# Performance work log

Measured on AMD Instinct MI355X. Metric: run time of the kernel, lower is better.

The kernel has to match this reference:

```python
import jax, jax.numpy as jnp
import numpy as np

N_NODES = 20000
IN_DIM = 256
HID = 128
N_CLASSES = 64
N_EDGES = 320000
EPS_BN = 1e-5


def setup_inputs() -> dict:
    key = jax.random.key(0)
    ks = jax.random.split(key, 24)
    s = 0.1
    inp = {}
    inp['x'] = jax.random.normal(ks[0], (N_NODES, IN_DIM), dtype=jnp.float32)
    inp['edge_index'] = jax.random.randint(ks[1], (2, N_EDGES), 0, N_NODES, dtype=jnp.int32)
    # GATConv 1: in=IN_DIM, out=HID per head, heads=4, concat=False
    inp['W1'] = s * jax.random.normal(ks[2], (IN_DIM, 4 * HID), dtype=jnp.float32)
    inp['a_src1'] = s * jax.random.normal(ks[3], (4, HID), dtype=jnp.float32)
    inp['a_dst1'] = s * jax.random.normal(ks[4], (4, HID), dtype=jnp.float32)
    inp['b1'] = jnp.zeros((HID,), jnp.float32)
    # GATConv 2: in=HID, out=HID per head, heads=4, concat=False
    inp['W2'] = s * jax.random.normal(ks[5], (HID, 4 * HID), dtype=jnp.float32)
    inp['a_src2'] = s * jax.random.normal(ks[6], (4, HID), dtype=jnp.float32)
    inp['a_dst2'] = s * jax.random.normal(ks[7], (4, HID), dtype=jnp.float32)
    inp['b2'] = jnp.zeros((HID,), jnp.float32)
    # GATConv 3: heads=1, concat=True (default)
    inp['W3'] = s * jax.random.normal(ks[8], (HID, HID), dtype=jnp.float32)
    inp['a_src3'] = s * jax.random.normal(ks[9], (1, HID), dtype=jnp.float32)
    inp['a_dst3'] = s * jax.random.normal(ks[10], (1, HID), dtype=jnp.float32)
    inp['b3'] = jnp.zeros((HID,), jnp.float32)
    # BatchNorm (eval-mode running stats)
    for i, k in zip((1, 2), (ks[11], ks[12])):
        inp[f'bn{i}_g'] = jnp.ones((HID,), jnp.float32)
        inp[f'bn{i}_b'] = jnp.zeros((HID,), jnp.float32)
        inp[f'bn{i}_m'] = 0.01 * jax.random.normal(k, (HID,), dtype=jnp.float32)
        inp[f'bn{i}_v'] = jnp.ones((HID,), jnp.float32)
    # classifier MLP
    inp['l1_w'] = s * jax.random.normal(ks[13], (HID, HID), dtype=jnp.float32)
    inp['l1_b'] = jnp.zeros((HID,), jnp.float32)
    inp['l2_w'] = s * jax.random.normal(ks[14], (HID, HID // 2), dtype=jnp.float32)
    inp['l2_b'] = jnp.zeros((HID // 2,), jnp.float32)
    inp['l3_w'] = s * jax.random.normal(ks[15], (HID // 2, N_CLASSES), dtype=jnp.float32)
    inp['l3_b'] = jnp.zeros((N_CLASSES,), jnp.float32)
    return inp


def _gat(x, src, dst, W, a_src, a_dst, b, heads, out_ch, concat):
    """PyG GATConv (with self-loops already appended to src/dst)."""
    n = x.shape[0]
    h = (x @ W).reshape(n, heads, out_ch)            # [N,H,C]
    alpha_s = jnp.sum(h * a_src[None], axis=-1)       # [N,H]
    alpha_d = jnp.sum(h * a_dst[None], axis=-1)       # [N,H]
    e = jax.nn.leaky_relu(alpha_s[src] + alpha_d[dst], 0.2)  # [E,H]
    # segment softmax over incoming edges of each destination node
    m = jax.ops.segment_max(e, dst, num_segments=n)
    m = jnp.where(jnp.isfinite(m), m, 0.0)
    ex = jnp.exp(e - m[dst])
    den = jax.ops.segment_sum(ex, dst, num_segments=n)
    alpha = ex / (den[dst] + 1e-16)                   # [E,H]
    msg = h[src] * alpha[:, :, None]                  # [E,H,C]
    out = jax.ops.segment_sum(msg, dst, num_segments=n)  # [N,H,C]
    out = out.reshape(n, heads * out_ch) if concat else out.mean(axis=1)
    return out + b


def _bn_eval(x, g, b, m, v):
    return g * (x - m) * jax.lax.rsqrt(v + EPS_BN) + b


def reference(x, edge_index, W1, a_src1, a_dst1, b1, W2, a_src2, a_dst2, b2,
              W3, a_src3, a_dst3, b3, bn1_g, bn1_b, bn1_m, bn1_v,
              bn2_g, bn2_b, bn2_m, bn2_v, l1_w, l1_b, l2_w, l2_b, l3_w, l3_b):
    n = x.shape[0]
    loops = jnp.arange(n, dtype=edge_index.dtype)
    src = jnp.concatenate([edge_index[0], loops])
    dst = jnp.concatenate([edge_index[1], loops])

    h = _gat(x, src, dst, W1, a_src1, a_dst1, b1, 4, HID, False)
    h = jax.nn.relu(_bn_eval(h, bn1_g, bn1_b, bn1_m, bn1_v))
    h = _gat(h, src, dst, W2, a_src2, a_dst2, b2, 4, HID, False)
    h = jax.nn.relu(_bn_eval(h, bn2_g, bn2_b, bn2_m, bn2_v))
    h = _gat(h, src, dst, W3, a_src3, a_dst3, b3, 1, HID, True)

    h = jax.nn.relu(h @ l1_w + l1_b)
    h = jax.nn.relu(h @ l2_w + l2_b)
    return jax.nn.sigmoid(h @ l3_w + l3_b)  # [N, num_labels]
```

## Files before the change

### kernel.cpp

```cpp
#include <hip/hip_runtime.h>
#include <cstdint>
#include <cstddef>

#define NN 20000

typedef __bf16 bf16_t;
typedef __bf16 bf16x8 __attribute__((ext_vector_type(8)));
typedef float f32x4 __attribute__((ext_vector_type(4)));

#define AS1 __attribute__((address_space(1)))
#define AS3 __attribute__((address_space(3)))

__device__ __forceinline__ float lrelu(float x) { return x >= 0.f ? x : 0.2f * x; }
__device__ __forceinline__ float bflo(uint32_t u) { return __uint_as_float(u << 16); }
__device__ __forceinline__ float bfhi(uint32_t u) { return __uint_as_float(u & 0xffff0000u); }

__device__ __forceinline__ uint32_t pack2bf(float a, float b) {
  bf16_t x = (bf16_t)a, y = (bf16_t)b;
  uint16_t ux = __builtin_bit_cast(uint16_t, x);
  uint16_t uy = __builtin_bit_cast(uint16_t, y);
  return (uint32_t)ux | ((uint32_t)uy << 16);
}


__global__ __launch_bounds__(1024) void scan_kernel(const int* __restrict__ cnt,
                                                    int* __restrict__ row_ptr,
                                                    int* __restrict__ cursor, int n) {
  __shared__ int wsum[16];
  const int t = threadIdx.x;
  const int lane = t & 63, w = t >> 6;
  int carry = 0;
  for (int base = 0; base < n; base += 1024) {
    int i = base + t;
    int v = (i < n) ? cnt[i] : 0;
    int x = v;
#pragma unroll
    for (int d = 1; d < 64; d <<= 1) {
      int y = __shfl_up(x, d);
      if (lane >= d) x += y;
    }
    if (lane == 63) wsum[w] = x;
    __syncthreads();
    if (t < 16) {
      int s = wsum[t];
#pragma unroll
      for (int d = 1; d < 16; d <<= 1) {
        int y = __shfl_up(s, d);
        if (t >= d) s += y;
      }
      wsum[t] = s;
    }
    __syncthreads();
    int blocksum = wsum[15];
    int wprefix = (w == 0) ? 0 : wsum[w - 1];
    int excl = carry + wprefix + (x - v);
    if (i < n) { row_ptr[i] = excl; cursor[i] = excl; }
    carry += blocksum;
    __syncthreads();
  }
  if (t == 0) row_ptr[n] = carry;
}


struct WDesc { const float* W; bf16_t* Bt; int K; int Cw; int H; float scale; int b0; };
struct WPack { WDesc d[4]; };

struct Prep1Args {
  WPack wp;
  const float *W1, *as1, *ad1, *W2, *as2, *ad2, *W3, *as3, *ad3;
  float *P1, *P2, *P3;
  const float *W3m, *L1w, *b3v, *l1b;
  bf16_t* M3t; float* bm;
  const int* ei; int E, N, EB;
  int* cnt;
};

__global__ __launch_bounds__(256) void prep1(Prep1Args a) {
  __shared__ float tile[32][33];
  const int b = blockIdx.x;
  const int t = threadIdx.x;

  if (b < 204) {
    int i = 3;
#pragma unroll
    for (int k = 2; k >= 0; --k)
      if (b < a.wp.d[k + 1].b0) i = k;
    const WDesc de = a.wp.d[i];
    const int bi = b - de.b0;
    const int ktiles = de.K / 32;
    const int kt = bi % ktiles, rt = bi / ktiles;
    const int gc = rt * 32;
    const int h = gc / de.Cw, c0 = gc % de.Cw;
    const int tx = t & 31, ty = t >> 5;
#pragma unroll
    for (int r = 0; r < 32; r += 8)
      tile[ty + r][tx] = de.W[(size_t)(kt * 32 + ty + r) * (de.H * de.Cw) + h * de.Cw + c0 + tx];
    __syncthreads();
#pragma unroll
    for (int r = 0; r < 32; r += 8)
      de.Bt[(size_t)(c0 + ty + r) * (de.H * de.K) + h * de.K + kt * 32 + tx] =
          (bf16_t)(de.scale * tile[tx][ty + r]);
  } else if (b < 716) {
    const int kk = b - 204;
    const float *W, *asrc, *adst;
    float* P;
    int K, H, k;
    if (kk < 256)      { W = a.W1; asrc = a.as1; adst = a.ad1; P = a.P1; K = 256; H = 4; k = kk; }
    else if (kk < 384) { W = a.W2; asrc = a.as2; adst = a.ad2; P = a.P2; K = 128; H = 4; k = kk - 256; }
    else               { W = a.W3; asrc = a.as3; adst = a.ad3; P = a.P3; K = 128; H = 1; k = kk - 384; }
    for (int j = 0; j < 2 * H; ++j) {
      const int h = (j < H) ? j : j - H;
      const float* av = (j < H) ? asrc : adst;
      float pv = 0.f;
      if (t < 128) pv = W[(size_t)k * (H * 128) + h * 128 + t] * av[h * 128 + t];
#pragma unroll
      for (int d = 1; d < 64; d <<= 1) pv += __shfl_xor(pv, d);
      if (t == 0 || t == 64) tile[0][t >> 6] = pv;
      __syncthreads();
      if (t == 0) P[j * K + k] = tile[0][0] + tile[0][1];
      __syncthreads();
    }
  } else if (b < 780) {
    const int idx = (b - 716) * 256 + t;
    const int k = idx >> 7, c = idx & 127;
    float s = 0.f;
    for (int m = 0; m < 128; ++m) s += a.W3m[k * 128 + m] * a.L1w[m * 128 + c];
    a.M3t[c * 128 + k] = (bf16_t)s;
    if (k == 0) {
      float tt = a.l1b[c];
      for (int m = 0; m < 128; ++m) tt += a.b3v[m] * a.L1w[m * 128 + c];
      a.bm[c] = tt;
    }
  } else {
    const int i = (b - 780) * 256 + t;
    if (i < a.E + a.N) {
      int dst = (i < a.E) ? a.ei[a.E + i] : (i - a.E);
      atomicAdd(&a.cnt[dst], 1);
    }
  }
}


__global__ __launch_bounds__(256) void scatter_cast(const int* __restrict__ ei, int E, int N,
                                                    int EB, int* __restrict__ cursor,
                                                    int* __restrict__ col,
                                                    const float* __restrict__ x,
                                                    const float* __restrict__ P1,
                                                    bf16_t* __restrict__ xb,
                                                    float* __restrict__ asadA) {
  const int b = blockIdx.x, t = threadIdx.x;
  if (b < EB) {
    const int i = b * 256 + t;
    if (i < E + N) {
      int src, dst;
      if (i < E) { src = ei[i]; dst = ei[E + i]; }
      else       { src = i - E; dst = src; }
      int slot = atomicAdd(&cursor[dst], 1);
      col[slot] = src;
    }
  } else {
    const int wv = t >> 6, lane = t & 63;
    const int n = (b - EB) * 4 + wv;
    const float4 v = *(const float4*)&x[(size_t)n * 256 + lane * 4];
    uint2 ov;
    ov.x = pack2bf(v.x, v.y);
    ov.y = pack2bf(v.z, v.w);
    *(uint2*)&xb[(size_t)n * 256 + lane * 4] = ov;
    float s[8];
#pragma unroll
    for (int j = 0; j < 8; ++j) {
      const float4 pj = *(const float4*)&P1[j * 256 + lane * 4];
      s[j] = v.x * pj.x + v.y * pj.y + v.z * pj.z + v.w * pj.w;
    }
#pragma unroll
    for (int j = 0; j < 8; ++j)
#pragma unroll
      for (int d = 1; d < 64; d <<= 1) s[j] += __shfl_xor(s[j], d);
    if (lane == 0) {
#pragma unroll
      for (int j = 0; j < 8; ++j) asadA[(size_t)n * 8 + j] = s[j];
    }
  }
}


template <int TN, int ACT, typename OUT_T>
__global__ __launch_bounds__(256) void gemm_mfma(const bf16_t* __restrict__ A,
                                                 const bf16_t* __restrict__ Bt,
                                                 const float* __restrict__ bias,
                                                 const float* __restrict__ bng,
                                                 const float* __restrict__ bnb,
                                                 const float* __restrict__ bnm,
                                                 const float* __restrict__ bnv,
                                                 OUT_T* __restrict__ C,
                                                 int M, int N, int K) {
  constexpr int TM = 128, BK = 64;
  constexpr int MT = (TN == 128) ? 4 : 2;
  constexpr int NRB = (TN * BK * 2) / 4096;
  __shared__ __align__(16) bf16_t As[TM * BK];
  __shared__ __align__(16) bf16_t Bs[TN * BK];

  const int t = threadIdx.x;
  const int wave = t >> 6, lane = t & 63;
  const int ln15 = lane & 15, quad = lane >> 4;
  const int bm = blockIdx.x * TM;
  const int bn = blockIdx.y * TN;
  const int wm = (TN == 128) ? (wave >> 1) * 64 : wave * 32;
  const int wn = (TN == 128) ? (wave & 1) * 64 : 0;
  const int rowLimA = M - 1 - bm;
  const size_t strideAB = (size_t)K * 2;

  f32x4 acc[MT][4];
#pragma unroll
  for (int mi = 0; mi < MT; ++mi)
#pragma unroll
    for (int ni = 0; ni < 4; ++ni) acc[mi][ni] = (f32x4){0.f, 0.f, 0.f, 0.f};

  const char* gA = (const char*)(A + (size_t)bm * K);
  const char* gB = (const char*)(Bt + (size_t)bn * K);

  for (int k0 = 0; k0 < K; k0 += BK) {
#pragma unroll
    for (int r = 0; r < 4; ++r) {
      int base = (wave * 4 + r) * 1024;
      int flat = base + lane * 16;
      int row = flat >> 7;
      int grow = row < rowLimA ? row : rowLimA;
      const char* gp = gA + (size_t)grow * strideAB + (size_t)(k0 * 2) + (flat & 127);
      __builtin_amdgcn_global_load_lds((const AS1 void*)gp,
                                       (AS3 void*)((char*)As + base), 16, 0, 0);
    }
#pragma unroll
    for (int r = 0; r < NRB; ++r) {
      int base = (wave * NRB + r) * 1024;
      int flat = base + lane * 16;
      int row = flat >> 7;
      const char* gp = gB + (size_t)row * strideAB + (size_t)(k0 * 2) + (flat & 127);
      __builtin_amdgcn_global_load_lds((const AS1 void*)gp,
                                       (AS3 void*)((char*)Bs + base), 16, 0, 0);
    }
    __syncthreads();
#pragma unroll
    for (int kk = 0; kk < BK; kk += 32) {
      bf16x8 af[MT], bfr[4];
#pragma unroll
      for (int mi = 0; mi < MT; ++mi)
        af[mi] = *(const bf16x8*)&As[(wm + mi * 16 + ln15) * BK + kk + quad * 8];
#pragma unroll
      for (int ni = 0; ni < 4; ++ni)
        bfr[ni] = *(const bf16x8*)&Bs[(wn + ni * 16 + ln15) * BK + kk + quad * 8];
#pragma unroll
      for (int mi = 0; mi < MT; ++mi)
#pragma unroll
        for (int ni = 0; ni < 4; ++ni)
          acc[mi][ni] = __builtin_amdgcn_mfma_f32_16x16x32_bf16(af[mi], bfr[ni], acc[mi][ni], 0, 0, 0);
    }
    __syncthreads();
  }

#pragma unroll
  for (int mi = 0; mi < MT; ++mi) {
    int r0 = bm + wm + mi * 16 + quad * 4;
#pragma unroll
    for (int ni = 0; ni < 4; ++ni) {
      int c = bn + wn + ni * 16 + ln15;
      float bv = bias ? bias[c] : 0.f;
      float sc = 1.f, sh = 0.f;
      if (ACT == 3) {
        sc = bng[c] * rsqrtf(bnv[c] + 1e-5f);
        sh = bnb[c] - bnm[c] * sc;
      }
#pragma unroll
      for (int reg = 0; reg < 4; ++reg) {
        int r = r0 + reg;
        if (r < M) {
          float v = acc[mi][ni][reg] + bv;
          if (ACT == 1) v = fmaxf(v, 0.f);
          else if (ACT == 3) v = fmaxf(v * sc + sh, 0.f);
          C[(size_t)r * N + c] = (OUT_T)v;
        }
      }
    }
  }
}


template <int K, int H>
__global__ __launch_bounds__(256) void alpha_gemm(const bf16_t* __restrict__ f,
                                                  const float* __restrict__ P,
                                                  float* __restrict__ asad) {
  constexpr int J = 2 * H;
  constexpr int KC = K / 64;
  const int wv = threadIdx.x >> 6, lane = threadIdx.x & 63;
  const int n = blockIdx.x * 4 + wv;
  float v[KC];
  if (KC == 4) {
    uint2 pv = *(const uint2*)&f[(size_t)n * K + lane * 4];
    v[0] = bflo(pv.x); v[1] = bfhi(pv.x); v[2] = bflo(pv.y); v[3] = bfhi(pv.y);
  } else {
    uint32_t pv = *(const uint32_t*)&f[(size_t)n * K + lane * 2];
    v[0] = bflo(pv); v[1] = bfhi(pv);
  }
  float s[J];
#pragma unroll
  for (int j = 0; j < J; ++j) {
    float acc = 0.f;
#pragma unroll
    for (int q = 0; q < KC; ++q) acc += v[q] * P[j * K + lane * KC + q];
    s[j] = acc;
  }
#pragma unroll
  for (int j = 0; j < J; ++j)
#pragma unroll
    for (int d = 1; d < 64; d <<= 1) s[j] += __shfl_xor(s[j], d);
  if (lane == 0) {
#pragma unroll
    for (int j = 0; j < J; ++j) asad[(size_t)n * J + j] = s[j];
  }
}


template <int K>
__global__ __launch_bounds__(128) void gat_agg_in4(const bf16_t* __restrict__ f,
                                                   const float* __restrict__ asad,
                                                   const int* __restrict__ rp,
                                                   const int* __restrict__ cs,
                                                   bf16_t* __restrict__ agg) {
  constexpr int KC = K / 64;
  const int wv = threadIdx.x >> 6, lane = threadIdx.x & 63;
  const int n = blockIdx.x * 2 + wv;
  __shared__ int sb[2][64];
  __shared__ float4 wl[2][64];

  const int r0 = rp[n], r1 = rp[n + 1];
  const int deg = r1 - r0;
  const float4 adv = *(const float4*)&asad[(size_t)n * 8 + 4];
  const char* fb = (const char*)f;
  const size_t loff = (size_t)lane * (KC * 2);

  float acc[4][KC];
#pragma unroll
  for (int j = 0; j < 4; ++j)
#pragma unroll
    for (int q = 0; q < KC; ++q) acc[j][q] = 0.f;

  auto edge_fma = [&](const char* gp, float4 w4) {
    if (KC == 4) {
      uint2 b = *(const uint2*)gp;
      float v0 = bflo(b.x), v1 = bfhi(b.x), v2 = bflo(b.y), v3 = bfhi(b.y);
      acc[0][0] += w4.x * v0; acc[0][1] += w4.x * v1; acc[0][2] += w4.x * v2; acc[0][3] += w4.x * v3;
      acc[1][0] += w4.y * v0; acc[1][1] += w4.y * v1; acc[1][2] += w4.y * v2; acc[1][3] += w4.y * v3;
      acc[2][0] += w4.z * v0; acc[2][1] += w4.z * v1; acc[2][2] += w4.z * v2; acc[2][3] += w4.z * v3;
      acc[3][0] += w4.w * v0; acc[3][1] += w4.w * v1; acc[3][2] += w4.w * v2; acc[3][3] += w4.w * v3;
    } else {
      uint32_t b = *(const uint32_t*)gp;
      float v0 = bflo(b), v1 = bfhi(b);
      acc[0][0] += w4.x * v0; acc[0][1] += w4.x * v1;
      acc[1][0] += w4.y * v0; acc[1][1] += w4.y * v1;
      acc[2][0] += w4.z * v0; acc[2][1] += w4.z * v1;
      acc[3][0] += w4.w * v0; acc[3][1] += w4.w * v1;
    }
  };

  if (deg <= 64) {
    const bool valid = lane < deg;
    int s = 0;
    float e0 = -1e30f, e1 = -1e30f, e2 = -1e30f, e3 = -1e30f;
    if (valid) {
      s = cs[r0 + lane];
      const float4 av = *(const float4*)&asad[(size_t)s * 8];
      e0 = lrelu(av.x + adv.x); e1 = lrelu(av.y + adv.y);
      e2 = lrelu(av.z + adv.z); e3 = lrelu(av.w + adv.w);
    }
    float m0 = e0, m1 = e1, m2 = e2, m3 = e3;
#pragma unroll
    for (int d = 1; d < 64; d <<= 1) {
      m0 = fmaxf(m0, __shfl_xor(m0, d)); m1 = fmaxf(m1, __shfl_xor(m1, d));
      m2 = fmaxf(m2, __shfl_xor(m2, d)); m3 = fmaxf(m3, __shfl_xor(m3, d));
    }
    float x0 = valid ? __expf(e0 - m0) : 0.f;
    float x1 = valid ? __expf(e1 - m1) : 0.f;
    float x2 = valid ? __expf(e2 - m2) : 0.f;
    float x3 = valid ? __expf(e3 - m3) : 0.f;
    float d0 = x0, d1 = x1, d2 = x2, d3 = x3;
#pragma unroll
    for (int d = 1; d < 64; d <<= 1) {
      d0 += __shfl_xor(d0, d); d1 += __shfl_xor(d1, d);
      d2 += __shfl_xor(d2, d); d3 += __shfl_xor(d3, d);
    }
    if (valid) {
      sb[wv][lane] = s * (K * 2);
      wl[wv][lane] = make_float4(x0 / (d0 + 1e-16f), x1 / (d1 + 1e-16f),
                                 x2 / (d2 + 1e-16f), x3 / (d3 + 1e-16f));
    }
    __builtin_amdgcn_wave_barrier();

    int g = 0;
    for (; g + 8 <= deg; g += 8) {
      const char* p[8];
      float4 w[8];
#pragma unroll
      for (int k = 0; k < 8; ++k) { p[k] = fb + (size_t)sb[wv][g + k] + loff; w[k] = wl[wv][g + k]; }
      if (KC == 4) {
        uint2 b[8];
#pragma unroll
        for (int k = 0; k < 8; ++k) b[k] = *(const uint2*)p[k];
#pragma unroll
        for (int k = 0; k < 8; ++k) {
          float v0 = bflo(b[k].x), v1 = bfhi(b[k].x), v2 = bflo(b[k].y), v3 = bfhi(b[k].y);
          acc[0][0] += w[k].x * v0; acc[0][1] += w[k].x * v1; acc[0][2] += w[k].x * v2; acc[0][3] += w[k].x * v3;
          acc[1][0] += w[k].y * v0; acc[1][1] += w[k].y * v1; acc[1][2] += w[k].y * v2; acc[1][3] += w[k].y * v3;
          acc[2][0] += w[k].z * v0; acc[2][1] += w[k].z * v1; acc[2][2] += w[k].z * v2; acc[2][3] += w[k].z * v3;
          acc[3][0] += w[k].w * v0; acc[3][1] += w[k].w * v1; acc[3][2] += w[k].w * v2; acc[3][3] += w[k].w * v3;
        }
      } else {
        uint32_t b[8];
#pragma unroll
        for (int k = 0; k < 8; ++k) b[k] = *(const uint32_t*)p[k];
#pragma unroll
        for (int k = 0; k < 8; ++k) {
          float v0 = bflo(b[k]), v1 = bfhi(b[k]);
          acc[0][0] += w[k].x * v0; acc[0][1] += w[k].x * v1;
          acc[1][0] += w[k].y * v0; acc[1][1] += w[k].y * v1;
          acc[2][0] += w[k].z * v0; acc[2][1] += w[k].z * v1;
          acc[3][0] += w[k].w * v0; acc[3][1] += w[k].w * v1;
        }
      }
    }
    for (; g < deg; ++g)
      edge_fma(fb + (size_t)sb[wv][g] + loff, wl[wv][g]);
  } else {
    float m0 = -1e30f, m1 = -1e30f, m2 = -1e30f, m3 = -1e30f;
    for (int i = r0 + lane; i < r1; i += 64) {
      const float4 av = *(const float4*)&asad[(size_t)cs[i] * 8];
      m0 = fmaxf(m0, lrelu(av.x + adv.x)); m1 = fmaxf(m1, lrelu(av.y + adv.y));
      m2 = fmaxf(m2, lrelu(av.z + adv.z)); m3 = fmaxf(m3, lrelu(av.w + adv.w));
    }
#pragma unroll
    for (int d = 1; d < 64; d <<= 1) {
      m0 = fmaxf(m0, __shfl_xor(m0, d)); m1 = fmaxf(m1, __shfl_xor(m1, d));
      m2 = fmaxf(m2, __shfl_xor(m2, d)); m3 = fmaxf(m3, __shfl_xor(m3, d));
    }
    float d0 = 0.f, d1 = 0.f, d2 = 0.f, d3 = 0.f;
    for (int i = r0 + lane; i < r1; i += 64) {
      const float4 av = *(const float4*)&asad[(size_t)cs[i] * 8];
      d0 += __expf(lrelu(av.x + adv.x) - m0); d1 += __expf(lrelu(av.y + adv.y) - m1);
      d2 += __expf(lrelu(av.z + adv.z) - m2); d3 += __expf(lrelu(av.w + adv.w) - m3);
    }
#pragma unroll
    for (int d = 1; d < 64; d <<= 1) {
      d0 += __shfl_xor(d0, d); d1 += __shfl_xor(d1, d);
      d2 += __shfl_xor(d2, d); d3 += __shfl_xor(d3, d);
    }
    const float i0 = 1.f / (d0 + 1e-16f), i1 = 1.f / (d1 + 1e-16f);
    const float i2 = 1.f / (d2 + 1e-16f), i3 = 1.f / (d3 + 1e-16f);
    for (int base = r0; base < r1; base += 64) {
      const int ne = min(64, r1 - base);
      if (lane < ne) {
        const int s = cs[base + lane];
        const float4 av = *(const float4*)&asad[(size_t)s * 8];
        sb[wv][lane] = s * (K * 2);
        wl[wv][lane] = make_float4(__expf(lrelu(av.x + adv.x) - m0) * i0,
                                   __expf(lrelu(av.y + adv.y) - m1) * i1,
                                   __expf(lrelu(av.z + adv.z) - m2) * i2,
                                   __expf(lrelu(av.w + adv.w) - m3) * i3);
      }
      __builtin_amdgcn_wave_barrier();
      for (int g = 0; g < ne; ++g)
        edge_fma(fb + (size_t)sb[wv][g] + loff, wl[wv][g]);
      __builtin_amdgcn_wave_barrier();
    }
  }

#pragma unroll
  for (int j = 0; j < 4; ++j) {
    if (KC == 4) {
      uint2 ov;
      ov.x = pack2bf(acc[j][0], acc[j][1]);
      ov.y = pack2bf(acc[j][2], acc[j][3]);
      *(uint2*)&agg[(size_t)n * (4 * K) + j * K + lane * 4] = ov;
    } else {
      *(uint32_t*)&agg[(size_t)n * (4 * K) + j * K + lane * 2] = pack2bf(acc[j][0], acc[j][1]);
    }
  }
}


__global__ __launch_bounds__(128) void gat_agg_in1(const bf16_t* __restrict__ f,
                                                   const float* __restrict__ asad,
                                                   const int* __restrict__ rp,
                                                   const int* __restrict__ cs,
                                                   bf16_t* __restrict__ agg) {
  const int wv = threadIdx.x >> 6, lane = threadIdx.x & 63;
  const int n = blockIdx.x * 2 + wv;
  __shared__ int sb[2][64];
  __shared__ float wl[2][64];

  const int r0 = rp[n], r1 = rp[n + 1];
  const int deg = r1 - r0;
  const float adv = asad[(size_t)n * 2 + 1];
  const char* fb = (const char*)f;
  const size_t loff = (size_t)lane * 4;
  float a0 = 0.f, a1 = 0.f;

  auto fma2 = [&](uint32_t v, float w) { a0 += w * bflo(v); a1 += w * bfhi(v); };

  if (deg <= 64) {
    const bool valid = lane < deg;
    int s = 0;
    float e = -1e30f;
    if (valid) { s = cs[r0 + lane]; e = lrelu(asad[(size_t)s * 2] + adv); }
    float m = e;
#pragma unroll
    for (int d = 1; d < 64; d <<= 1) m = fmaxf(m, __shfl_xor(m, d));
    float x = valid ? __expf(e - m) : 0.f;
    float den = x;
#pragma unroll
    for (int d = 1; d < 64; d <<= 1) den += __shfl_xor(den, d);
    if (valid) { sb[wv][lane] = s * 256; wl[wv][lane] = x / (den + 1e-16f); }
    __builtin_amdgcn_wave_barrier();
    int g = 0;
    for (; g + 8 <= deg; g += 8) {
      uint32_t b[8];
      float w[8];
#pragma unroll
      for (int k = 0; k < 8; ++k) {
        b[k] = *(const uint32_t*)(fb + (size_t)sb[wv][g + k] + loff);
        w[k] = wl[wv][g + k];
      }
#pragma unroll
      for (int k = 0; k < 8; ++k) { a0 += w[k] * bflo(b[k]); a1 += w[k] * bfhi(b[k]); }
    }
    for (; g < deg; ++g)
      fma2(*(const uint32_t*)(fb + (size_t)sb[wv][g] + loff), wl[wv][g]);
  } else {
    float m = -1e30f;
    for (int i = r0 + lane; i < r1; i += 64) m = fmaxf(m, lrelu(asad[(size_t)cs[i] * 2] + adv));
#pragma unroll
    for (int d = 1; d < 64; d <<= 1) m = fmaxf(m, __shfl_xor(m, d));
    float den = 0.f;
    for (int i = r0 + lane; i < r1; i += 64) den += __expf(lrelu(asad[(size_t)cs[i] * 2] + adv) - m);
#pragma unroll
    for (int d = 1; d < 64; d <<= 1) den += __shfl_xor(den, d);
    const float dinv = 1.f / (den + 1e-16f);
    for (int base = r0; base < r1; base += 64) {
      const int ne = min(64, r1 - base);
      if (lane < ne) {
        const int s = cs[base + lane];
        sb[wv][lane] = s * 256;
        wl[wv][lane] = __expf(lrelu(asad[(size_t)s * 2] + adv) - m) * dinv;
      }
      __builtin_amdgcn_wave_barrier();
      for (int g = 0; g < ne; ++g)
        fma2(*(const uint32_t*)(fb + (size_t)sb[wv][g] + loff), wl[wv][g]);
      __builtin_amdgcn_wave_barrier();
    }
  }
  *(uint32_t*)&agg[(size_t)n * 128 + lane * 2] = pack2bf(a0, a1);
}


__global__ __launch_bounds__(256) void mlp_tail(const bf16_t* __restrict__ A,
                                                const bf16_t* __restrict__ M3t,
                                                const float* __restrict__ bm,
                                                const bf16_t* __restrict__ l2t,
                                                const float* __restrict__ l2b,
                                                const bf16_t* __restrict__ l3t,
                                                const float* __restrict__ l3b,
                                                float* __restrict__ out, int M) {
  __shared__ __align__(16) bf16_t As[128 * 128];
  __shared__ __align__(16) bf16_t Ws[128 * 128];
  const int t = threadIdx.x, wave = t >> 6, lane = t & 63;
  const int ln15 = lane & 15, quad = lane >> 4;
  const int bmr = blockIdx.x * 128;
  const int rowLim = M - 1 - bmr;

#pragma unroll
  for (int r = 0; r < 8; ++r) {
    int base = (wave * 8 + r) * 1024;
    int flat = base + lane * 16;
    int row = flat >> 8;
    int grow = row < rowLim ? row : rowLim;
    const char* gp = (const char*)A + (size_t)grow * 256 + (flat & 255);
    __builtin_amdgcn_global_load_lds((const AS1 void*)gp,
                                     (AS3 void*)((char*)As + base), 16, 0, 0);
  }
#pragma unroll
  for (int r = 0; r < 8; ++r) {
    int base = (wave * 8 + r) * 1024;
    __builtin_amdgcn_global_load_lds((const AS1 void*)((const char*)M3t + base + lane * 16),
                                     (AS3 void*)((char*)Ws + base), 16, 0, 0);
  }
  __syncthreads();

  const int wm = wave * 32;
  f32x4 a1[2][8];
#pragma unroll
  for (int mi = 0; mi < 2; ++mi)
#pragma unroll
    for (int ni = 0; ni < 8; ++ni) a1[mi][ni] = (f32x4){0.f, 0.f, 0.f, 0.f};
#pragma unroll
  for (int kk = 0; kk < 128; kk += 32) {
    bf16x8 af[2];
#pragma unroll
    for (int mi = 0; mi < 2; ++mi)
      af[mi] = *(const bf16x8*)&As[(wm + mi * 16 + ln15) * 128 + kk + quad * 8];
#pragma unroll
    for (int ni = 0; ni < 8; ++ni) {
      bf16x8 bf = *(const bf16x8*)&Ws[(ni * 16 + ln15) * 128 + kk + quad * 8];
#pragma unroll
      for (int mi = 0; mi < 2; ++mi)
        a1[mi][ni] = __builtin_amdgcn_mfma_f32_16x16x32_bf16(af[mi], bf, a1[mi][ni], 0, 0, 0);
    }
  }
  __syncthreads();

#pragma unroll
  for (int r = 0; r < 4; ++r) {
    int base = (wave * 4 + r) * 1024;
    __builtin_amdgcn_global_load_lds((const AS1 void*)((const char*)l2t + base + lane * 16),
                                     (AS3 void*)((char*)Ws + base), 16, 0, 0);
  }
#pragma unroll
  for (int r = 0; r < 2; ++r) {
    int base = (wave * 2 + r) * 1024;
    __builtin_amdgcn_global_load_lds((const AS1 void*)((const char*)l3t + base + lane * 16),
                                     (AS3 void*)((char*)Ws + 8192 * 2 + base), 16, 0, 0);
  }
#pragma unroll
  for (int mi = 0; mi < 2; ++mi) {
    int r0 = wm + mi * 16 + quad * 4;
#pragma unroll
    for (int ni = 0; ni < 8; ++ni) {
      int c = ni * 16 + ln15;
      float bv = bm[c];
#pragma unroll
      for (int reg = 0; reg < 4; ++reg)
        As[(r0 + reg) * 128 + c] = (bf16_t)fmaxf(a1[mi][ni][reg] + bv, 0.f);
    }
  }
  __syncthreads();

  f32x4 a2[2][4];
#pragma unroll
  for (int mi = 0; mi < 2; ++mi)
#pragma unroll
    for (int ni = 0; ni < 4; ++ni) a2[mi][ni] = (f32x4){0.f, 0.f, 0.f, 0.f};
#pragma unroll
  for (int kk = 0; kk < 128; kk += 32) {
    bf16x8 af[2];
#pragma unroll
    for (int mi = 0; mi < 2; ++mi)
      af[mi] = *(const bf16x8*)&As[(wm + mi * 16 + ln15) * 128 + kk + quad * 8];
#pragma unroll
    for (int ni = 0; ni < 4; ++ni) {
      bf16x8 bf = *(const bf16x8*)&Ws[(ni * 16 + ln15) * 128 + kk + quad * 8];
#pragma unroll
      for (int mi = 0; mi < 2; ++mi)
        a2[mi][ni] = __builtin_amdgcn_mfma_f32_16x16x32_bf16(af[mi], bf, a2[mi][ni], 0, 0, 0);
    }
  }
  __syncthreads();

#pragma unroll
  for (int mi = 0; mi < 2; ++mi) {
    int r0 = wm + mi * 16 + quad * 4;
#pragma unroll
    for (int ni = 0; ni < 4; ++ni) {
      int c = ni * 16 + ln15;
      float bv = l2b[c];
#pragma unroll
      for (int reg = 0; reg < 4; ++reg)
        As[(r0 + reg) * 64 + c] = (bf16_t)fmaxf(a2[mi][ni][reg] + bv, 0.f);
    }
  }
  __syncthreads();

  f32x4 a3[2][4];
#pragma unroll
  for (int mi = 0; mi < 2; ++mi)
#pragma unroll
    for (int ni = 0; ni < 4; ++ni) a3[mi][ni] = (f32x4){0.f, 0.f, 0.f, 0.f};
#pragma unroll
  for (int kk = 0; kk < 64; kk += 32) {
    bf16x8 af[2];
#pragma unroll
    for (int mi = 0; mi < 2; ++mi)
      af[mi] = *(const bf16x8*)&As[(wm + mi * 16 + ln15) * 64 + kk + quad * 8];
#pragma unroll
    for (int ni = 0; ni < 4; ++ni) {
      bf16x8 bf = *(const bf16x8*)&Ws[8192 + (ni * 16 + ln15) * 64 + kk + quad * 8];
#pragma unroll
      for (int mi = 0; mi < 2; ++mi)
        a3[mi][ni] = __builtin_amdgcn_mfma_f32_16x16x32_bf16(af[mi], bf, a3[mi][ni], 0, 0, 0);
    }
  }
#pragma unroll
  for (int mi = 0; mi < 2; ++mi) {
    int r0 = wm + mi * 16 + quad * 4;
#pragma unroll
    for (int ni = 0; ni < 4; ++ni) {
      int c = ni * 16 + ln15;
      float bv = l3b[c];
#pragma unroll
      for (int reg = 0; reg < 4; ++reg) {
        int r = bmr + r0 + reg;
        if (r < M) {
          float v = a3[mi][ni][reg] + bv;
          out[(size_t)r * 64 + c] = 1.f / (1.f + __expf(-v));
        }
      }
    }
  }
}


extern "C" void kernel_launch(void* const* d_in, const int* in_sizes, int n_in,
                              void* d_out, int out_size, void* d_ws, size_t ws_size,
                              hipStream_t stream) {
  const float* x      = (const float*)d_in[0];
  const int*   ei     = (const int*)d_in[1];
  const float* W1     = (const float*)d_in[2];
  const float* a_src1 = (const float*)d_in[3];
  const float* a_dst1 = (const float*)d_in[4];
  const float* b1     = (const float*)d_in[5];
  const float* W2     = (const float*)d_in[6];
  const float* a_src2 = (const float*)d_in[7];
  const float* a_dst2 = (const float*)d_in[8];
  const float* b2     = (const float*)d_in[9];
  const float* W3     = (const float*)d_in[10];
  const float* a_src3 = (const float*)d_in[11];
  const float* a_dst3 = (const float*)d_in[12];
  const float* b3     = (const float*)d_in[13];
  const float* bn1g = (const float*)d_in[14];
  const float* bn1b = (const float*)d_in[15];
  const float* bn1m = (const float*)d_in[16];
  const float* bn1v = (const float*)d_in[17];
  const float* bn2g = (const float*)d_in[18];
  const float* bn2b = (const float*)d_in[19];
  const float* bn2m = (const float*)d_in[20];
  const float* bn2v = (const float*)d_in[21];
  const float* l1w = (const float*)d_in[22];
  const float* l1b = (const float*)d_in[23];
  const float* l2w = (const float*)d_in[24];
  const float* l2b = (const float*)d_in[25];
  const float* l3w = (const float*)d_in[26];
  const float* l3b = (const float*)d_in[27];
  float* out = (float*)d_out;

  const int N = NN;
  const int E = in_sizes[1] / 2;
  const int ET = E + N;
  const int EB = (ET + 255) / 256;

  char* p = (char*)d_ws;
  auto carve = [&](size_t bytes) {
    char* q = p;
    p += (bytes + 255) & ~(size_t)255;
    return q;
  };
  bf16_t* xb    = (bf16_t*)carve((size_t)N * 256 * 2);
  bf16_t* aggb  = (bf16_t*)carve((size_t)N * 1024 * 2);
  bf16_t* f1b   = (bf16_t*)carve((size_t)N * 128 * 2);
  bf16_t* f2b   = (bf16_t*)carve((size_t)N * 128 * 2);
  float* asadA  = (float*)carve((size_t)N * 8 * 4);
  float* asadB  = (float*)carve((size_t)N * 8 * 4);
  float* asadC  = (float*)carve((size_t)N * 2 * 4);
  int* cnt      = (int*)carve((size_t)N * 4);
  int* cursor   = (int*)carve((size_t)N * 4);
  int* row_ptr  = (int*)carve((size_t)(N + 1) * 4);
  int* col      = (int*)carve((size_t)ET * 4);
  bf16_t* Ws1t  = (bf16_t*)carve((size_t)128 * 1024 * 2);
  bf16_t* Ws2t  = (bf16_t*)carve((size_t)128 * 512 * 2);
  bf16_t* M3t   = (bf16_t*)carve((size_t)128 * 128 * 2);
  bf16_t* l2t   = (bf16_t*)carve((size_t)64 * 128 * 2);
  bf16_t* l3t   = (bf16_t*)carve((size_t)64 * 64 * 2);
  float* P1     = (float*)carve((size_t)8 * 256 * 4);
  float* P2     = (float*)carve((size_t)8 * 128 * 4);
  float* P3     = (float*)carve((size_t)2 * 128 * 4);
  float* bm     = (float*)carve((size_t)128 * 4);
  (void)ws_size; (void)n_in; (void)out_size;

  hipMemsetAsync(cnt, 0, (size_t)N * 4, stream);

  Prep1Args pa;
  pa.wp.d[0] = {W1,  Ws1t, 256, 128, 4, 0.25f, 0};
  pa.wp.d[1] = {W2,  Ws2t, 128, 128, 4, 0.25f, 128};
  pa.wp.d[2] = {l2w, l2t,  128, 64,  1, 1.0f,  192};
  pa.wp.d[3] = {l3w, l3t,  64,  64,  1, 1.0f,  200};
  pa.W1 = W1; pa.as1 = a_src1; pa.ad1 = a_dst1;
  pa.W2 = W2; pa.as2 = a_src2; pa.ad2 = a_dst2;
  pa.W3 = W3; pa.as3 = a_src3; pa.ad3 = a_dst3;
  pa.P1 = P1; pa.P2 = P2; pa.P3 = P3;
  pa.W3m = W3; pa.L1w = l1w; pa.b3v = b3; pa.l1b = l1b;
  pa.M3t = M3t; pa.bm = bm;
  pa.ei = ei; pa.E = E; pa.N = N; pa.EB = EB;
  pa.cnt = cnt;
  prep1<<<780 + EB, 256, 0, stream>>>(pa);

  scan_kernel<<<1, 1024, 0, stream>>>(cnt, row_ptr, cursor, N);
  scatter_cast<<<EB + N / 4, 256, 0, stream>>>(ei, E, N, EB, cursor, col, x, P1, xb, asadA);

  const int gm = (N + 127) / 128;
  const int ab = N / 4;
  const int gb = N / 2;

  gat_agg_in4<256><<<gb, 128, 0, stream>>>(xb, asadA, row_ptr, col, aggb);
  gemm_mfma<64, 3, bf16_t><<<dim3(gm, 2), 256, 0, stream>>>(
      aggb, Ws1t, b1, bn1g, bn1b, bn1m, bn1v, f1b, N, 128, 1024);

  alpha_gemm<128, 4><<<ab, 256, 0, stream>>>(f1b, P2, asadB);
  gat_agg_in4<128><<<gb, 128, 0, stream>>>(f1b, asadB, row_ptr, col, aggb);
  gemm_mfma<64, 3, bf16_t><<<dim3(gm, 2), 256, 0, stream>>>(
      aggb, Ws2t, b2, bn2g, bn2b, bn2m, bn2v, f2b, N, 128, 512);

  alpha_gemm<128, 1><<<ab, 256, 0, stream>>>(f2b, P3, asadC);
  gat_agg_in1<<<gb, 128, 0, stream>>>(f2b, asadC, row_ptr, col, aggb);
  mlp_tail<<<gm, 256, 0, stream>>>(aggb, M3t, bm, l2t, l2b, l3t, l3b, out, N);
}
```

Baseline: 334.0 us.

## Replace CSR build with fixed-capacity adjacency buckets and fuse attention scores into GEMM

Replaces the count, scan and scatter CSR construction with per-destination buckets of fixed capacity (CAP=96). Edges are written directly during the counting pass in prep1, which removes the scan kernel and the separate scatter pass. The attention-score projections (alpha_gemm) are folded into the GEMM epilogue: partial dot products are reduced across the wave and atomically accumulated into zero-initialised asad buffers, which removes two more launches and a re-read of the features. The risks are out-of-bounds writes if any node's in-degree exceeds the capacity, a larger and sparser col array, and atomic contention on the score buffers.

```diff
diff --git a/kernel.cpp b/kernel.cpp
--- a/kernel.cpp
+++ b/kernel.cpp
@@ -3,6 +3,7 @@
 #include <cstddef>
 
 #define NN 20000
+#define CAP 96
 
 typedef __bf16 bf16_t;
 typedef __bf16 bf16x8 __attribute__((ext_vector_type(8)));
@@ -20,45 +21,6 @@
   uint16_t ux = __builtin_bit_cast(uint16_t, x);
   uint16_t uy = __builtin_bit_cast(uint16_t, y);
   return (uint32_t)ux | ((uint32_t)uy << 16);
-}
-
-
-__global__ __launch_bounds__(1024) void scan_kernel(const int* __restrict__ cnt,
-                                                    int* __restrict__ row_ptr,
-                                                    int* __restrict__ cursor, int n) {
-  __shared__ int wsum[16];
-  const int t = threadIdx.x;
-  const int lane = t & 63, w = t >> 6;
-  int carry = 0;
-  for (int base = 0; base < n; base += 1024) {
-    int i = base + t;
-    int v = (i < n) ? cnt[i] : 0;
-    int x = v;
-#pragma unroll
-    for (int d = 1; d < 64; d <<= 1) {
-      int y = __shfl_up(x, d);
-      if (lane >= d) x += y;
-    }
-    if (lane == 63) wsum[w] = x;
-    __syncthreads();
-    if (t < 16) {
-      int s = wsum[t];
-#pragma unroll
-      for (int d = 1; d < 16; d <<= 1) {
-        int y = __shfl_up(s, d);
-        if (t >= d) s += y;
-      }
-      wsum[t] = s;
-    }
-    __syncthreads();
-    int blocksum = wsum[15];
-    int wprefix = (w == 0) ? 0 : wsum[w - 1];
-    int excl = carry + wprefix + (x - v);
-    if (i < n) { row_ptr[i] = excl; cursor[i] = excl; }
-    carry += blocksum;
-    __syncthreads();
-  }
-  if (t == 0) row_ptr[n] = carry;
 }
 
 
@@ -72,7 +34,7 @@
   const float *W3m, *L1w, *b3v, *l1b;
   bf16_t* M3t; float* bm;
   const int* ei; int E, N, EB;
-  int* cnt;
+  int* cnt; int* col;
 };
 
 __global__ __launch_bounds__(256) void prep1(Prep1Args a) {
@@ -134,57 +96,46 @@
   } else {
     const int i = (b - 780) * 256 + t;
     if (i < a.E + a.N) {
-      int dst = (i < a.E) ? a.ei[a.E + i] : (i - a.E);
-      atomicAdd(&a.cnt[dst], 1);
+      int src, dst;
+      if (i < a.E) { src = a.ei[i]; dst = a.ei[a.E + i]; }
+      else         { src = i - a.E; dst = src; }
+      int slot = atomicAdd(&a.cnt[dst], 1);
+      a.col[(size_t)dst * CAP + slot] = src;
     }
   }
 }
 
 
-__global__ __launch_bounds__(256) void scatter_cast(const int* __restrict__ ei, int E, int N,
-                                                    int EB, int* __restrict__ cursor,
-                                                    int* __restrict__ col,
-                                                    const float* __restrict__ x,
-                                                    const float* __restrict__ P1,
-                                                    bf16_t* __restrict__ xb,
-                                                    float* __restrict__ asadA) {
+__global__ __launch_bounds__(256) void cast_alpha(const float* __restrict__ x,
+                                                  const float* __restrict__ P1,
+                                                  bf16_t* __restrict__ xb,
+                                                  float* __restrict__ asadA) {
   const int b = blockIdx.x, t = threadIdx.x;
-  if (b < EB) {
-    const int i = b * 256 + t;
-    if (i < E + N) {
-      int src, dst;
-      if (i < E) { src = ei[i]; dst = ei[E + i]; }
-      else       { src = i - E; dst = src; }
-      int slot = atomicAdd(&cursor[dst], 1);
-      col[slot] = src;
-    }
-  } else {
-    const int wv = t >> 6, lane = t & 63;
-    const int n = (b - EB) * 4 + wv;
-    const float4 v = *(const float4*)&x[(size_t)n * 256 + lane * 4];
-    uint2 ov;
-    ov.x = pack2bf(v.x, v.y);
-    ov.y = pack2bf(v.z, v.w);
-    *(uint2*)&xb[(size_t)n * 256 + lane * 4] = ov;
-    float s[8];
-#pragma unroll
-    for (int j = 0; j < 8; ++j) {
-      const float4 pj = *(const float4*)&P1[j * 256 + lane * 4];
-      s[j] = v.x * pj.x + v.y * pj.y + v.z * pj.z + v.w * pj.w;
-    }
-#pragma unroll
-    for (int j = 0; j < 8; ++j)
-#pragma unroll
-      for (int d = 1; d < 64; d <<= 1) s[j] += __shfl_xor(s[j], d);
-    if (lane == 0) {
-#pragma unroll
-      for (int j = 0; j < 8; ++j) asadA[(size_t)n * 8 + j] = s[j];
-    }
+  const int wv = t >> 6, lane = t & 63;
+  const int n = b * 4 + wv;
+  const float4 v = *(const float4*)&x[(size_t)n * 256 + lane * 4];
+  uint2 ov;
+  ov.x = pack2bf(v.x, v.y);
+  ov.y = pack2bf(v.z, v.w);
+  *(uint2*)&xb[(size_t)n * 256 + lane * 4] = ov;
+  float s[8];
+#pragma unroll
+  for (int j = 0; j < 8; ++j) {
+    const float4 pj = *(const float4*)&P1[j * 256 + lane * 4];
+    s[j] = v.x * pj.x + v.y * pj.y + v.z * pj.z + v.w * pj.w;
+  }
+#pragma unroll
+  for (int j = 0; j < 8; ++j)
+#pragma unroll
+    for (int d = 1; d < 64; d <<= 1) s[j] += __shfl_xor(s[j], d);
+  if (lane == 0) {
+#pragma unroll
+    for (int j = 0; j < 8; ++j) asadA[(size_t)n * 8 + j] = s[j];
   }
 }
 
 
-template <int TN, int ACT, typename OUT_T>
+template <int TN, int ACT, int J, typename OUT_T>
 __global__ __launch_bounds__(256) void gemm_mfma(const bf16_t* __restrict__ A,
                                                  const bf16_t* __restrict__ Bt,
                                                  const float* __restrict__ bias,
@@ -193,6 +144,8 @@
                                                  const float* __restrict__ bnm,
                                                  const float* __restrict__ bnv,
                                                  OUT_T* __restrict__ C,
+                                                 const float* __restrict__ Pa,
+                                                 float* __restrict__ asad,
                                                  int M, int N, int K) {
   constexpr int TM = 128, BK = 64;
   constexpr int MT = (TN == 128) ? 4 : 2;
@@ -273,49 +226,46 @@
 #pragma unroll
       for (int reg = 0; reg < 4; ++reg) {
         int r = r0 + reg;
-        if (r < M) {
-          float v = acc[mi][ni][reg] + bv;
-          if (ACT == 1) v = fmaxf(v, 0.f);
-          else if (ACT == 3) v = fmaxf(v * sc + sh, 0.f);
-          C[(size_t)r * N + c] = (OUT_T)v;
-        }
+        float v = acc[mi][ni][reg] + bv;
+        if (ACT == 1) v = fmaxf(v, 0.f);
+        else if (ACT == 3) v = fmaxf(v * sc + sh, 0.f);
+        acc[mi][ni][reg] = v;
+        if (r < M) C[(size_t)r * N + c] = (OUT_T)v;
       }
     }
   }
-}
-
-
-template <int K, int H>
-__global__ __launch_bounds__(256) void alpha_gemm(const bf16_t* __restrict__ f,
-                                                  const float* __restrict__ P,
-                                                  float* __restrict__ asad) {
-  constexpr int J = 2 * H;
-  constexpr int KC = K / 64;
-  const int wv = threadIdx.x >> 6, lane = threadIdx.x & 63;
-  const int n = blockIdx.x * 4 + wv;
-  float v[KC];
-  if (KC == 4) {
-    uint2 pv = *(const uint2*)&f[(size_t)n * K + lane * 4];
-    v[0] = bflo(pv.x); v[1] = bfhi(pv.x); v[2] = bflo(pv.y); v[3] = bfhi(pv.y);
-  } else {
-    uint32_t pv = *(const uint32_t*)&f[(size_t)n * K + lane * 2];
-    v[0] = bflo(pv); v[1] = bfhi(pv);
-  }
-  float s[J];
-#pragma unroll
-  for (int j = 0; j < J; ++j) {
-    float acc = 0.f;
-#pragma unroll
-    for (int q = 0; q < KC; ++q) acc += v[q] * P[j * K + lane * KC + q];
-    s[j] = acc;
-  }
-#pragma unroll
-  for (int j = 0; j < J; ++j)
-#pragma unroll
-    for (int d = 1; d < 64; d <<= 1) s[j] += __shfl_xor(s[j], d);
-  if (lane == 0) {
-#pragma unroll
-    for (int j = 0; j < J; ++j) asad[(size_t)n * J + j] = s[j];
+
+  if (J > 0) {
+#pragma unroll
+    for (int j = 0; j < J; ++j) {
+      float pj[4];
+#pragma unroll
+      for (int ni = 0; ni < 4; ++ni)
+        pj[ni] = Pa[j * 128 + bn + wn + ni * 16 + ln15];
+      float s[MT][4];
+#pragma unroll
+      for (int mi = 0; mi < MT; ++mi)
+#pragma unroll
+        for (int reg = 0; reg < 4; ++reg)
+          s[mi][reg] = acc[mi][0][reg] * pj[0] + acc[mi][1][reg] * pj[1] +
+                       acc[mi][2][reg] * pj[2] + acc[mi][3][reg] * pj[3];
+#pragma unroll
+      for (int d = 1; d < 16; d <<= 1)
+#pragma unroll
+        for (int mi = 0; mi < MT; ++mi)
+#pragma unroll
+          for (int reg = 0; reg < 4; ++reg)
+            s[mi][reg] += __shfl_xor(s[mi][reg], d);
+      if (ln15 == 0) {
+#pragma unroll
+        for (int mi = 0; mi < MT; ++mi)
+#pragma unroll
+          for (int reg = 0; reg < 4; ++reg) {
+            int r = bm + wm + mi * 16 + quad * 4 + reg;
+            if (r < M) atomicAdd(&asad[(size_t)r * J + j], s[mi][reg]);
+          }
+      }
+    }
   }
 }
 
@@ -323,8 +273,8 @@
 template <int K>
 __global__ __launch_bounds__(128) void gat_agg_in4(const bf16_t* __restrict__ f,
                                                    const float* __restrict__ asad,
-                                                   const int* __restrict__ rp,
-                                                   const int* __restrict__ cs,
+                                                   const int* __restrict__ cnt,
+                                                   const int* __restrict__ col,
                                                    bf16_t* __restrict__ agg) {
   constexpr int KC = K / 64;
   const int wv = threadIdx.x >> 6, lane = threadIdx.x & 63;
@@ -332,8 +282,9 @@
   __shared__ int sb[2][64];
   __shared__ float4 wl[2][64];
 
-  const int r0 = rp[n], r1 = rp[n + 1];
-  const int deg = r1 - r0;
+  const int r0 = n * CAP;
+  const int deg = cnt[n];
+  const int r1 = r0 + deg;
   const float4 adv = *(const float4*)&asad[(size_t)n * 8 + 4];
   const char* fb = (const char*)f;
   const size_t loff = (size_t)lane * (KC * 2);
@@ -367,7 +318,7 @@
     int s = 0;
     float e0 = -1e30f, e1 = -1e30f, e2 = -1e30f, e3 = -1e30f;
     if (valid) {
-      s = cs[r0 + lane];
+      s = col[r0 + lane];
       const float4 av = *(const float4*)&asad[(size_t)s * 8];
       e0 = lrelu(av.x + adv.x); e1 = lrelu(av.y + adv.y);
       e2 = lrelu(av.z + adv.z); e3 = lrelu(av.w + adv.w);
@@ -432,7 +383,7 @@
   } else {
     float m0 = -1e30f, m1 = -1e30f, m2 = -1e30f, m3 = -1e30f;
     for (int i = r0 + lane; i < r1; i += 64) {
-      const float4 av = *(const float4*)&asad[(size_t)cs[i] * 8];
+      const float4 av = *(const float4*)&asad[(size_t)col[i] * 8];
       m0 = fmaxf(m0, lrelu(av.x + adv.x)); m1 = fmaxf(m1, lrelu(av.y + adv.y));
       m2 = fmaxf(m2, lrelu(av.z + adv.z)); m3 = fmaxf(m3, lrelu(av.w + adv.w));
     }
@@ -443,7 +394,7 @@
     }
     float d0 = 0.f, d1 = 0.f, d2 = 0.f, d3 = 0.f;
     for (int i = r0 + lane; i < r1; i += 64) {
-      const float4 av = *(const float4*)&asad[(size_t)cs[i] * 8];
+      const float4 av = *(const float4*)&asad[(size_t)col[i] * 8];
       d0 += __expf(lrelu(av.x + adv.x) - m0); d1 += __expf(lrelu(av.y + adv.y) - m1);
       d2 += __expf(lrelu(av.z + adv.z) - m2); d3 += __expf(lrelu(av.w + adv.w) - m3);
     }
@@ -457,7 +408,7 @@
     for (int base = r0; base < r1; base += 64) {
       const int ne = min(64, r1 - base);
       if (lane < ne) {
-        const int s = cs[base + lane];
+        const int s = col[base + lane];
         const float4 av = *(const float4*)&asad[(size_t)s * 8];
         sb[wv][lane] = s * (K * 2);
         wl[wv][lane] = make_float4(__expf(lrelu(av.x + adv.x) - m0) * i0,
@@ -488,16 +439,17 @@
 
 __global__ __launch_bounds__(128) void gat_agg_in1(const bf16_t* __restrict__ f,
                                                    const float* __restrict__ asad,
-                                                   const int* __restrict__ rp,
-                                                   const int* __restrict__ cs,
+                                                   const int* __restrict__ cnt,
+                                                   const int* __restrict__ col,
                                                    bf16_t* __restrict__ agg) {
   const int wv = threadIdx.x >> 6, lane = threadIdx.x & 63;
   const int n = blockIdx.x * 2 + wv;
   __shared__ int sb[2][64];
   __shared__ float wl[2][64];
 
-  const int r0 = rp[n], r1 = rp[n + 1];
-  const int deg = r1 - r0;
+  const int r0 = n * CAP;
+  const int deg = cnt[n];
+  const int r1 = r0 + deg;
   const float adv = asad[(size_t)n * 2 + 1];
   const char* fb = (const char*)f;
   const size_t loff = (size_t)lane * 4;
@@ -509,7 +461,7 @@
     const bool valid = lane < deg;
     int s = 0;
     float e = -1e30f;
-    if (valid) { s = cs[r0 + lane]; e = lrelu(asad[(size_t)s * 2] + adv); }
+    if (valid) { s = col[r0 + lane]; e = lrelu(asad[(size_t)s * 2] + adv); }
     float m = e;
 #pragma unroll
     for (int d = 1; d < 64; d <<= 1) m = fmaxf(m, __shfl_xor(m, d));
@@ -535,18 +487,18 @@
       fma2(*(const uint32_t*)(fb + (size_t)sb[wv][g] + loff), wl[wv][g]);
   } else {
     float m = -1e30f;
-    for (int i = r0 + lane; i < r1; i += 64) m = fmaxf(m, lrelu(asad[(size_t)cs[i] * 2] + adv));
+    for (int i = r0 + lane; i < r1; i += 64) m = fmaxf(m, lrelu(asad[(size_t)col[i] * 2] + adv));
 #pragma unroll
     for (int d = 1; d < 64; d <<= 1) m = fmaxf(m, __shfl_xor(m, d));
     float den = 0.f;
-    for (int i = r0 + lane; i < r1; i += 64) den += __expf(lrelu(asad[(size_t)cs[i] * 2] + adv) - m);
+    for (int i = r0 + lane; i < r1; i += 64) den += __expf(lrelu(asad[(size_t)col[i] * 2] + adv) - m);
 #pragma unroll
     for (int d = 1; d < 64; d <<= 1) den += __shfl_xor(den, d);
     const float dinv = 1.f / (den + 1e-16f);
     for (int base = r0; base < r1; base += 64) {
       const int ne = min(64, r1 - base);
       if (lane < ne) {
-        const int s = cs[base + lane];
+        const int s = col[base + lane];
         sb[wv][lane] = s * 256;
         wl[wv][lane] = __expf(lrelu(asad[(size_t)s * 2] + adv) - m) * dinv;
       }
@@ -764,12 +716,11 @@
   bf16_t* f1b   = (bf16_t*)carve((size_t)N * 128 * 2);
   bf16_t* f2b   = (bf16_t*)carve((size_t)N * 128 * 2);
   float* asadA  = (float*)carve((size_t)N * 8 * 4);
+  int* cnt      = (int*)carve((size_t)N * 4);
   float* asadB  = (float*)carve((size_t)N * 8 * 4);
   float* asadC  = (float*)carve((size_t)N * 2 * 4);
-  int* cnt      = (int*)carve((size_t)N * 4);
-  int* cursor   = (int*)carve((size_t)N * 4);
-  int* row_ptr  = (int*)carve((size_t)(N + 1) * 4);
-  int* col      = (int*)carve((size_t)ET * 4);
+  const size_t zbytes = (size_t)(p - (char*)cnt);
+  int* col      = (int*)carve((size_t)N * CAP * 4);
   bf16_t* Ws1t  = (bf16_t*)carve((size_t)128 * 1024 * 2);
   bf16_t* Ws2t  = (bf16_t*)carve((size_t)128 * 512 * 2);
   bf16_t* M3t   = (bf16_t*)carve((size_t)128 * 128 * 2);
@@ -781,7 +732,7 @@
   float* bm     = (float*)carve((size_t)128 * 4);
   (void)ws_size; (void)n_in; (void)out_size;
 
-  hipMemsetAsync(cnt, 0, (size_t)N * 4, stream);
+  hipMemsetAsync(cnt, 0, zbytes, stream);
 
   Prep1Args pa;
   pa.wp.d[0] = {W1,  Ws1t, 256, 128, 4, 0.25f, 0};
@@ -795,26 +746,22 @@
   pa.W3m = W3; pa.L1w = l1w; pa.b3v = b3; pa.l1b = l1b;
   pa.M3t = M3t; pa.bm = bm;
   pa.ei = ei; pa.E = E; pa.N = N; pa.EB = EB;
-  pa.cnt = cnt;
+  pa.cnt = cnt; pa.col = col;
   prep1<<<780 + EB, 256, 0, stream>>>(pa);
 
-  scan_kernel<<<1, 1024, 0, stream>>>(cnt, row_ptr, cursor, N);
-  scatter_cast<<<EB + N / 4, 256, 0, stream>>>(ei, E, N, EB, cursor, col, x, P1, xb, asadA);
+  cast_alpha<<<N / 4, 256, 0, stream>>>(x, P1, xb, asadA);
 
   const int gm = (N + 127) / 128;
-  const int ab = N / 4;
   const int gb = N / 2;
 
-  gat_agg_in4<256><<<gb, 128, 0, stream>>>(xb, asadA, row_ptr, col, aggb);
-  gemm_mfma<64, 3, bf16_t><<<dim3(gm, 2), 256, 0, stream>>>(
-      aggb, Ws1t, b1, bn1g, bn1b, bn1m, bn1v, f1b, N, 128, 1024);
-
-  alpha_gemm<128, 4><<<ab, 256, 0, stream>>>(f1b, P2, asadB);
-  gat_agg_in4<128><<<gb, 128, 0, stream>>>(f1b, asadB, row_ptr, col, aggb);
-  gemm_mfma<64, 3, bf16_t><<<dim3(gm, 2), 256, 0, stream>>>(
-      aggb, Ws2t, b2, bn2g, bn2b, bn2m, bn2v, f2b, N, 128, 512);
-
-  alpha_gemm<128, 1><<<ab, 256, 0, stream>>>(f2b, P3, asadC);
-  gat_agg_in1<<<gb, 128, 0, stream>>>(f2b, asadC, row_ptr, col, aggb);
+  gat_agg_in4<256><<<gb, 128, 0, stream>>>(xb, asadA, cnt, col, aggb);
+  gemm_mfma<64, 3, 8, bf16_t><<<dim3(gm, 2), 256, 0, stream>>>(
+      aggb, Ws1t, b1, bn1g, bn1b, bn1m, bn1v, f1b, P2, asadB, N, 128, 1024);
+
+  gat_agg_in4<128><<<gb, 128, 0, stream>>>(f1b, asadB, cnt, col, aggb);
+  gemm_mfma<64, 3, 2, bf16_t><<<dim3(gm, 2), 256, 0, stream>>>(
+      aggb, Ws2t, b2, bn2g, bn2b, bn2m, bn2v, f2b, P3, asadC, N, 128, 512);
+
+  gat_agg_in1<<<gb, 128, 0, stream>>>(f2b, asadC, cnt, col, aggb);
   mlp_tail<<<gm, 256, 0, stream>>>(aggb, M3t, bm, l2t, l2b, l3t, l3b, out, N);
 }
```

Measured after the change: 299.4 us. 10.4% less time.
